# Kernel tuning notes

Measured on AMD Instinct MI355X. Metric: run time of the kernel, lower is better.

## Reference

```python
import jax, jax.numpy as jnp
import numpy as np

B, H, N, D = 8, 12, 1024, 64
SCALE = 1.0 / float(np.sqrt(D))  # 0.125; torch forward default is 1.0 but 1/sqrt(d) is the production value
EPS = 1e-06


def setup_inputs() -> dict:
    key = jax.random.key(0)
    kq, kk, kv = jax.random.split(key, 3)
    q = jax.random.normal(kq, (B, H, N, D), dtype=jnp.float32)
    k = jax.random.normal(kk, (B, H, N, D), dtype=jnp.float32)
    v = jax.random.normal(kv, (B, H, N, D), dtype=jnp.float32)
    # Parameter init per L2Q.__init__: alpha=0.125, beta=0.5, gamma=1/n_tokens
    alpha = jnp.full((H, 1, 1), 0.125, dtype=jnp.float32)
    beta = jnp.full((H, 1, 1), 0.5, dtype=jnp.float32)
    gamma = jnp.full((H, 1, 1), 1.0 / N, dtype=jnp.float32)
    return {"q": q, "k": k, "v": v, "alpha": alpha, "beta": beta, "gamma": gamma}


def reference(q, k, v, alpha, beta, gamma):
    # logits: (B, H, N, N)
    logits = jnp.einsum("bhnd,bhmd->bhnm", q, k) * SCALE
    # per-head quadratic polynomial, then ReLU; params (H,1,1) broadcast over (B,H,N,N)
    attn = jax.nn.relu(alpha * logits * logits + beta * logits + gamma)
    attn = attn / (jnp.sum(attn, axis=-1, keepdims=True) + EPS)
    return jnp.einsum("bhnm,bhmd->bhnd", attn, v)
```

## Files before the change

kernel.cpp:

```cpp
#include <hip/hip_runtime.h>
#include <hip/hip_bf16.h>

typedef __attribute__((ext_vector_type(8))) short bf16x8;
typedef __attribute__((ext_vector_type(4))) float f32x4;
typedef __attribute__((ext_vector_type(16))) float f32x16;

#define MFMA16(a, b, c) __builtin_amdgcn_mfma_f32_16x16x32_bf16(a, b, c, 0, 0, 0)
#define MFMA32(a, b, c) __builtin_amdgcn_mfma_f32_32x32x16_bf16(a, b, c, 0, 0, 0)

static constexpr int kH = 12;
static constexpr int kN = 1024;
static constexpr int kD = 64;
static constexpr int kBH = 96;
static constexpr int kND = kN * kD;
static constexpr float kScale = 0.125f;
static constexpr float kEps = 1e-6f;
static constexpr long kTensorElems = (long)kBH * kND;
static constexpr long kWsNeeded = 2 * kTensorElems * 2;

__device__ __forceinline__ unsigned bfbits(float x) {
    union { __hip_bfloat16 h; unsigned short u; } c;
    c.h = __float2bfloat16(x);
    return (unsigned)c.u;
}
__device__ __forceinline__ unsigned pack2_rne(float a, float b) {
    return bfbits(a) | (bfbits(b) << 16);
}
__device__ __forceinline__ unsigned pack2_rhu(float lo, float hi) {
    unsigned a = __builtin_bit_cast(unsigned, lo) + 0x8000u;
    unsigned b = __builtin_bit_cast(unsigned, hi) + 0x8000u;
    return __builtin_amdgcn_perm(b, a, 0x07060302u);
}
__device__ __forceinline__ void gl_lds16(const void* g, void* l) {
    __builtin_amdgcn_global_load_lds(
        (const __attribute__((address_space(1))) void*)g,
        (__attribute__((address_space(3))) void*)l, 16, 0, 0);
}

__global__ __launch_bounds__(256, 2) void prep(
    const float* __restrict__ k, const float* __restrict__ v,
    unsigned* __restrict__ kbf, unsigned* __restrict__ vtb)
{
    static constexpr int TS = 68;
    __shared__ float T32[64 * TS];
    const int bid = blockIdx.x;
    const int bh = bid >> 4, nt = bid & 15;
    const int t = threadIdx.x;

    const float* kp = k + (long)bh * kND + (long)nt * 64 * kD;
    unsigned* ko = kbf + ((long)bh * kND + (long)nt * 64 * kD) / 2;
#pragma unroll
    for (int r = 0; r < 4; ++r) {
        const int f4 = t + 256 * r;
        const float4 f = ((const float4*)kp)[f4];
        uint2 u;
        u.x = pack2_rne(f.x, f.y);
        u.y = pack2_rne(f.z, f.w);
        *(uint2*)&ko[f4 * 2] = u;
    }

    const float* vp = v + (long)bh * kND + (long)nt * 64 * kD;
#pragma unroll
    for (int r = 0; r < 4; ++r) {
        const int f4 = t + 256 * r;
        const int n = f4 >> 4, d4 = f4 & 15;
        const float4 f = *(const float4*)(vp + (long)n * kD + 4 * d4);
        *(float4*)&T32[n * TS + 4 * d4] = f;
    }
    __syncthreads();
    const int d = t >> 2, c = t & 3;
    unsigned u[8];
#pragma unroll
    for (int j = 0; j < 8; ++j) {
        const int key = c * 16 + 2 * j;
        u[j] = pack2_rne(T32[key * TS + d], T32[(key + 1) * TS + d]);
    }
    unsigned* dst = vtb + (long)bh * (kND / 2) + (long)d * (kN / 2) + nt * 32 + c * 8;
    uint4 A, B;
    A.x = u[0]; A.y = u[1]; A.z = u[4]; A.w = u[5];
    B.x = u[2]; B.y = u[3]; B.z = u[6]; B.w = u[7];
    *(uint4*)(dst)     = A;
    *(uint4*)(dst + 4) = B;
}

__global__ __launch_bounds__(256, 3) void l2q_main(
    const float* __restrict__ q,
    const unsigned short* __restrict__ kbf, const unsigned short* __restrict__ vtbf,
    const float* __restrict__ alpha, const float* __restrict__ beta, const float* __restrict__ gamma,
    float* __restrict__ out)
{
    __shared__ __align__(16) unsigned Ks[2][2048];
    __shared__ __align__(16) unsigned Vs[2][2048];

    const int bid  = blockIdx.x;
    const int xcd  = bid & 7;
    const int sIdx = bid >> 3;
    const int bh   = xcd * 12 + (sIdx % 12);
    const int qt   = sIdx / 12;
    const int h    = bh % kH;
    const int t    = threadIdx.x;
    const int wave = t >> 6;
    const int lane = t & 63;
    const int l31  = lane & 31;
    const int hh   = lane >> 5;

    const float al = alpha[h] * (kScale * kScale);
    const float be = beta[h] * kScale;
    const float ga = gamma[h];

    const float* qp = q + (long)bh * kND;
    const unsigned short* kp = kbf + (long)bh * kND;
    const unsigned short* vp = vtbf + (long)bh * kND;

    bf16x8 qbF[4];
    {
        const int qrow = qt * 128 + wave * 32 + l31;
        const float* qsrc = qp + (long)qrow * kD;
#pragma unroll
        for (int s = 0; s < 4; ++s) {
            const float4 f0 = *(const float4*)(qsrc + s * 16 + hh * 8);
            const float4 f1 = *(const float4*)(qsrc + s * 16 + hh * 8 + 4);
            uint4 u;
            u.x = pack2_rne(f0.x, f0.y);
            u.y = pack2_rne(f0.z, f0.w);
            u.z = pack2_rne(f1.x, f1.y);
            u.w = pack2_rne(f1.z, f1.w);
            qbF[s] = __builtin_bit_cast(bf16x8, u);
        }
    }

    f32x16 oacc[2];
#pragma unroll
    for (int db = 0; db < 2; ++db)
#pragma unroll
        for (int r = 0; r < 16; ++r)
            oacc[db][r] = 0.f;
    float dacc[4] = {0.f, 0.f, 0.f, 0.f};

    const int srow8 = lane >> 3;
    const int g8    = lane & 7;
    auto stageKV = [&](int buf, int tile) {
        const int k0 = tile * 64;
#pragma unroll
        for (int c = 0; c < 2; ++c) {
            const int r = (c * 4 + wave) * 8 + srow8;
            gl_lds16(kp + (long)(k0 + r) * kD + (g8 ^ srow8) * 8, &Ks[buf][(c * 4 + wave) * 256]);
            gl_lds16(vp + (long)r * kN + k0 + (g8 ^ srow8) * 8, &Vs[buf][(c * 4 + wave) * 256]);
        }
    };

    stageKV(0, 0);

    for (int tile = 0; tile < 16; ++tile) {
        const int buf = tile & 1;
        __syncthreads();
        if (tile + 1 < 16) stageKV(buf ^ 1, tile + 1);

        const unsigned* Kb = Ks[buf];
        const unsigned* Vb = Vs[buf];

        f32x16 st[2];
#pragma unroll
        for (int kb = 0; kb < 2; ++kb)
#pragma unroll
            for (int r = 0; r < 16; ++r)
                st[kb][r] = 0.f;
#pragma unroll
        for (int s = 0; s < 4; ++s) {
            const int g = (s << 1) | hh;
#pragma unroll
            for (int kb = 0; kb < 2; ++kb) {
                const int row = kb * 32 + l31;
                bf16x8 ka = *(const bf16x8*)&Kb[row * 32 + ((g ^ (row & 7)) << 2)];
                st[kb] = MFMA32(ka, qbF[s], st[kb]);
            }
        }

        bf16x8 vfr[2][4];
#pragma unroll
        for (int db = 0; db < 2; ++db) {
            const int row = db * 32 + l31;
            const int rb = row * 32;
            const int rsw = row & 7;
#pragma unroll
            for (int s = 0; s < 4; ++s)
                vfr[db][s] = *(const bf16x8*)&Vb[rb + ((((s << 1) | hh) ^ rsw) << 2)];
        }

        unsigned u[2][8];
#pragma unroll
        for (int kb = 0; kb < 2; ++kb) {
#pragma unroll
            for (int p = 0; p < 8; ++p) {
                const float s0 = st[kb][2 * p], s1 = st[kb][2 * p + 1];
                const float w0 = fmaxf(fmaf(fmaf(al, s0, be), s0, ga), 0.f);
                const float w1 = fmaxf(fmaf(fmaf(al, s1, be), s1, ga), 0.f);
                dacc[p & 3] += w0 + w1;
                u[kb][p] = pack2_rhu(w0, w1);
            }
        }

#pragma unroll
        for (int s = 0; s < 4; ++s) {
            uint4 fr;
            const int kb = s >> 1, b = (s & 1) * 4;
            fr.x = u[kb][b + 0];
            fr.y = u[kb][b + 1];
            fr.z = u[kb][b + 2];
            fr.w = u[kb][b + 3];
            const bf16x8 pa = __builtin_bit_cast(bf16x8, fr);
            oacc[0] = MFMA32(pa, vfr[0][s], oacc[0]);
            oacc[1] = MFMA32(pa, vfr[1][s], oacc[1]);
        }
    }

    float d = (dacc[0] + dacc[1]) + (dacc[2] + dacc[3]);
    d += __shfl_xor(d, 32);
    const float inv = 1.0f / (d + kEps);

    const long obase = (long)bh * kND;
    const int rowbase = qt * 128 + wave * 32;
#pragma unroll
    for (int r = 0; r < 16; ++r) {
        const int row32 = (r & 3) + 8 * (r >> 2) + 4 * hh;
        const float iv = __shfl(inv, row32);
        float* o = out + obase + (long)(rowbase + row32) * kD + l31;
        o[0]  = oacc[0][r] * iv;
        o[32] = oacc[1][r] * iv;
    }
}

static constexpr int KSU = 36;
static constexpr int VSU = 36;
static constexpr int PSU = 36;

__global__ __launch_bounds__(256, 3) void l2q_attn_fb(
    const float* __restrict__ q, const float* __restrict__ k, const float* __restrict__ v,
    const float* __restrict__ alpha, const float* __restrict__ beta, const float* __restrict__ gamma,
    float* __restrict__ out)
{
    __shared__ __align__(16) unsigned KsU[64 * KSU];
    __shared__ __align__(16) unsigned VtU[64 * VSU];
    __shared__ __align__(16) unsigned PU[128 * PSU];

    const int bid  = blockIdx.x;
    const int bh   = bid >> 3;
    const int qt   = bid & 7;
    const int h    = bh % kH;
    const int t    = threadIdx.x;
    const int wave = t >> 6;
    const int lane = t & 63;
    const int quad = lane >> 4;
    const int l15  = lane & 15;

    const float al = alpha[h], be = beta[h], ga = gamma[h];

    const long base = (long)bh * kN * kD;
    const float* qp = q + base;
    const float* kp = k + base;
    const float* vp = v + base;

    bf16x8 qa[2][2];
#pragma unroll
    for (int rb = 0; rb < 2; ++rb) {
        const int row = qt * 128 + wave * 32 + rb * 16 + l15;
#pragma unroll
        for (int kc = 0; kc < 2; ++kc) {
            const float* src = qp + (long)row * kD + kc * 32 + quad * 8;
            const float4 f0 = *(const float4*)(src);
            const float4 f1 = *(const float4*)(src + 4);
            uint4 u;
            u.x = pack2_rne(f0.x, f0.y);
            u.y = pack2_rne(f0.z, f0.w);
            u.z = pack2_rne(f1.x, f1.y);
            u.w = pack2_rne(f1.z, f1.w);
            qa[rb][kc] = __builtin_bit_cast(bf16x8, u);
        }
    }

    f32x4 oacc[2][4];
#pragma unroll
    for (int rb = 0; rb < 2; ++rb)
#pragma unroll
        for (int db = 0; db < 4; ++db)
            oacc[rb][db] = (f32x4){0.f, 0.f, 0.f, 0.f};

    float dsum[2][4] = {{0.f, 0.f, 0.f, 0.f}, {0.f, 0.f, 0.f, 0.f}};
    unsigned* Pw = &PU[wave * 32 * PSU];

    for (int tile = 0; tile < 16; ++tile) {
        __syncthreads();
        const int k0 = tile * 64;
#pragma unroll
        for (int r = 0; r < 4; ++r) {
            const int f4 = t + 256 * r;
            const int n = f4 >> 4, d4 = f4 & 15;
            const float4 kg = *(const float4*)(kp + (long)(k0 + n) * kD + 4 * d4);
            uint2 pk;
            pk.x = pack2_rne(kg.x, kg.y);
            pk.y = pack2_rne(kg.z, kg.w);
            *(uint2*)&KsU[n * KSU + 2 * d4] = pk;
        }
#pragma unroll
        for (int r = 0; r < 2; ++r) {
            const int u = t + 256 * r;
            const int key2 = u & 31, d4 = u >> 5;
            const float* s0 = vp + (long)(k0 + 2 * key2) * kD + 4 * d4;
            const float4 va = *(const float4*)(s0);
            const float4 vb = *(const float4*)(s0 + kD);
            VtU[(4 * d4 + 0) * VSU + key2] = pack2_rne(va.x, vb.x);
            VtU[(4 * d4 + 1) * VSU + key2] = pack2_rne(va.y, vb.y);
            VtU[(4 * d4 + 2) * VSU + key2] = pack2_rne(va.z, vb.z);
            VtU[(4 * d4 + 3) * VSU + key2] = pack2_rne(va.w, vb.w);
        }
        __syncthreads();

        f32x4 s[2][4];
#pragma unroll
        for (int rb = 0; rb < 2; ++rb)
#pragma unroll
            for (int nb = 0; nb < 4; ++nb)
                s[rb][nb] = (f32x4){0.f, 0.f, 0.f, 0.f};
#pragma unroll
        for (int nb = 0; nb < 4; ++nb) {
            bf16x8 kb0 = *(const bf16x8*)&KsU[(nb * 16 + l15) * KSU + 4 * quad];
            bf16x8 kb1 = *(const bf16x8*)&KsU[(nb * 16 + l15) * KSU + 16 + 4 * quad];
#pragma unroll
            for (int rb = 0; rb < 2; ++rb) {
                s[rb][nb] = MFMA16(qa[rb][0], kb0, s[rb][nb]);
                s[rb][nb] = MFMA16(qa[rb][1], kb1, s[rb][nb]);
            }
        }

        const bool ev = (lane & 1) == 0;
#pragma unroll
        for (int rb = 0; rb < 2; ++rb) {
#pragma unroll
            for (int nb = 0; nb < 4; ++nb) {
                float w0, w1, w2, w3;
                {
                    float l0 = s[rb][nb][0] * kScale;
                    float l1 = s[rb][nb][1] * kScale;
                    float l2 = s[rb][nb][2] * kScale;
                    float l3 = s[rb][nb][3] * kScale;
                    w0 = fmaxf(fmaf(fmaf(al, l0, be), l0, ga), 0.f);
                    w1 = fmaxf(fmaf(fmaf(al, l1, be), l1, ga), 0.f);
                    w2 = fmaxf(fmaf(fmaf(al, l2, be), l2, ga), 0.f);
                    w3 = fmaxf(fmaf(fmaf(al, l3, be), l3, ga), 0.f);
                }
                dsum[rb][0] += w0; dsum[rb][1] += w1;
                dsum[rb][2] += w2; dsum[rb][3] += w3;

                const float o0 = __shfl_xor(w0, 1);
                const float o1 = __shfl_xor(w1, 1);
                const float o2 = __shfl_xor(w2, 1);
                const float o3 = __shfl_xor(w3, 1);
                const unsigned pa = ev ? pack2_rne(w0, o0) : pack2_rne(o2, w2);
                const unsigned pb = ev ? pack2_rne(w1, o1) : pack2_rne(o3, w3);
                const int r0 = ev ? 0 : 2;
                const int cu = (16 * nb + (l15 & ~1)) >> 1;
                const int rowb = rb * 16 + quad * 4 + r0;
                Pw[rowb * PSU + cu] = pa;
                Pw[(rowb + 1) * PSU + cu] = pb;
            }
        }

        bf16x8 pf[2][2];
#pragma unroll
        for (int rb = 0; rb < 2; ++rb)
#pragma unroll
            for (int kc = 0; kc < 2; ++kc)
                pf[rb][kc] = *(const bf16x8*)&Pw[(rb * 16 + l15) * PSU + 16 * kc + 4 * quad];
#pragma unroll
        for (int db = 0; db < 4; ++db) {
            bf16x8 vf0 = *(const bf16x8*)&VtU[(db * 16 + l15) * VSU + 4 * quad];
            bf16x8 vf1 = *(const bf16x8*)&VtU[(db * 16 + l15) * VSU + 16 + 4 * quad];
#pragma unroll
            for (int rb = 0; rb < 2; ++rb) {
                oacc[rb][db] = MFMA16(pf[rb][0], vf0, oacc[rb][db]);
                oacc[rb][db] = MFMA16(pf[rb][1], vf1, oacc[rb][db]);
            }
        }
    }

#pragma unroll
    for (int rb = 0; rb < 2; ++rb)
#pragma unroll
        for (int i = 0; i < 4; ++i) {
            float d = dsum[rb][i];
            d += __shfl_xor(d, 1);
            d += __shfl_xor(d, 2);
            d += __shfl_xor(d, 4);
            d += __shfl_xor(d, 8);
            dsum[rb][i] = 1.0f / (d + kEps);
        }

#pragma unroll
    for (int rb = 0; rb < 2; ++rb)
#pragma unroll
        for (int db = 0; db < 4; ++db)
#pragma unroll
            for (int i = 0; i < 4; ++i) {
                const int row = qt * 128 + wave * 32 + rb * 16 + quad * 4 + i;
                out[base + (long)row * kD + db * 16 + l15] = oacc[rb][db][i] * dsum[rb][i];
            }
}

extern "C" void kernel_launch(void* const* d_in, const int* in_sizes, int n_in,
                              void* d_out, int out_size, void* d_ws, size_t ws_size,
                              hipStream_t stream) {
    const float* q     = (const float*)d_in[0];
    const float* k     = (const float*)d_in[1];
    const float* v     = (const float*)d_in[2];
    const float* alpha = (const float*)d_in[3];
    const float* beta  = (const float*)d_in[4];
    const float* gamma = (const float*)d_in[5];
    float* out = (float*)d_out;

    if (ws_size < (size_t)kWsNeeded) {
        l2q_attn_fb<<<dim3(768), dim3(256), 0, stream>>>(q, k, v, alpha, beta, gamma, out);
        return;
    }

    unsigned* kbf = (unsigned*)d_ws;
    unsigned* vtb = kbf + kTensorElems / 2;

    prep<<<dim3(1536), dim3(256), 0, stream>>>(k, v, kbf, vtb);
    l2q_main<<<dim3(768), dim3(256), 0, stream>>>(
        q, (const unsigned short*)kbf, (const unsigned short*)vtb,
        alpha, beta, gamma, out);
}
```

Measured before the change: 144.3 us.

## Software-pipeline QK^T of next tile with PV of current tile

Restructures the key loop so the QK^T MFMAs for tile t+1 are issued right after the polynomial weights of tile t are formed, interleaved with that tile's PV MFMAs. V staging moves to a three-deep LDS buffer, and loads are prefetched two tiles ahead while K stays double-buffered. The loop is wrapped in s_setprio to favour the MFMA-heavy section. The aim is to hide the dependency between the score MFMAs and the elementwise/pack work, and to hide load latency. In exchange it uses more LDS (extra V buffer) and keeps the score accumulators live across iterations, which raises register pressure.

```diff
diff --git a/kernel.cpp b/kernel.cpp
--- a/kernel.cpp
+++ b/kernel.cpp
@@ -90,7 +90,7 @@
     float* __restrict__ out)
 {
     __shared__ __align__(16) unsigned Ks[2][2048];
-    __shared__ __align__(16) unsigned Vs[2][2048];
+    __shared__ __align__(16) unsigned Vs[3][2048];
 
     const int bid  = blockIdx.x;
     const int xcd  = bid & 7;
@@ -139,27 +139,26 @@
 
     const int srow8 = lane >> 3;
     const int g8    = lane & 7;
-    auto stageKV = [&](int buf, int tile) {
+    auto stageKV = [&](int tile) {
+        const int kbuf = tile & 1;
+        const int vbuf = tile % 3;
         const int k0 = tile * 64;
 #pragma unroll
         for (int c = 0; c < 2; ++c) {
-            const int r = (c * 4 + wave) * 8 + srow8;
-            gl_lds16(kp + (long)(k0 + r) * kD + (g8 ^ srow8) * 8, &Ks[buf][(c * 4 + wave) * 256]);
-            gl_lds16(vp + (long)r * kN + k0 + (g8 ^ srow8) * 8, &Vs[buf][(c * 4 + wave) * 256]);
+            const int seg = c * 4 + wave;
+            const int r = seg * 8 + srow8;
+            gl_lds16(kp + (long)(k0 + r) * kD + (g8 ^ srow8) * 8, &Ks[kbuf][seg * 256]);
+            gl_lds16(vp + (long)r * kN + k0 + (g8 ^ srow8) * 8, &Vs[vbuf][seg * 256]);
         }
     };
 
-    stageKV(0, 0);
-
-    for (int tile = 0; tile < 16; ++tile) {
-        const int buf = tile & 1;
-        __syncthreads();
-        if (tile + 1 < 16) stageKV(buf ^ 1, tile + 1);
-
-        const unsigned* Kb = Ks[buf];
-        const unsigned* Vb = Vs[buf];
-
-        f32x16 st[2];
+    stageKV(0);
+    stageKV(1);
+    __syncthreads();
+
+    f32x16 st[2];
+    {
+        const unsigned* Kb = Ks[0];
 #pragma unroll
         for (int kb = 0; kb < 2; ++kb)
 #pragma unroll
@@ -175,7 +174,13 @@
                 st[kb] = MFMA32(ka, qbF[s], st[kb]);
             }
         }
-
+    }
+
+    for (int tile = 0; tile < 16; ++tile) {
+        __syncthreads();
+        if (tile + 2 < 16) stageKV(tile + 2);
+
+        const unsigned* Vb = Vs[tile % 3];
         bf16x8 vfr[2][4];
 #pragma unroll
         for (int db = 0; db < 2; ++db) {
@@ -197,6 +202,26 @@
                 const float w1 = fmaxf(fmaf(fmaf(al, s1, be), s1, ga), 0.f);
                 dacc[p & 3] += w0 + w1;
                 u[kb][p] = pack2_rhu(w0, w1);
+            }
+        }
+
+        __builtin_amdgcn_s_setprio(1);
+        if (tile + 1 < 16) {
+            const unsigned* Kb = Ks[(tile + 1) & 1];
+#pragma unroll
+            for (int kb = 0; kb < 2; ++kb)
+#pragma unroll
+                for (int r = 0; r < 16; ++r)
+                    st[kb][r] = 0.f;
+#pragma unroll
+            for (int s = 0; s < 4; ++s) {
+                const int g = (s << 1) | hh;
+#pragma unroll
+                for (int kb = 0; kb < 2; ++kb) {
+                    const int row = kb * 32 + l31;
+                    bf16x8 ka = *(const bf16x8*)&Kb[row * 32 + ((g ^ (row & 7)) << 2)];
+                    st[kb] = MFMA32(ka, qbF[s], st[kb]);
+                }
             }
         }
 
@@ -212,6 +237,7 @@
             oacc[0] = MFMA32(pa, vfr[0][s], oacc[0]);
             oacc[1] = MFMA32(pa, vfr[1][s], oacc[1]);
         }
+        __builtin_amdgcn_s_setprio(0);
     }
 
     float d = (dacc[0] + dacc[1]) + (dacc[2] + dacc[3]);
```

After: 152.6 us. 5.8% more time.

## Pre-swizzle V into MFMA fragment layout and load directly from global

Applied to the files above, without the earlier changes.

The V-transpose prep kernel now writes V^T in a fragment-ordered layout, so each lane's bf16x8 MFMA operand is contiguous in global memory. The main kernel drops the V LDS double buffer and loads V fragments straight from global (L2) into registers at the start of each tile, before the QK MFMAs. This removes LDS staging traffic and LDS footprint for V, which could raise occupancy. The cost is exposed global-load latency inside the loop, with no async prefetch beyond issuing the loads before the score computation.

```diff
diff --git a/kernel.cpp b/kernel.cpp
--- a/kernel.cpp
+++ b/kernel.cpp
@@ -75,12 +75,13 @@
         const int key = c * 16 + 2 * j;
         u[j] = pack2_rne(T32[key * TS + d], T32[(key + 1) * TS + d]);
     }
-    unsigned* dst = vtb + (long)bh * (kND / 2) + (long)d * (kN / 2) + nt * 32 + c * 8;
     uint4 A, B;
     A.x = u[0]; A.y = u[1]; A.z = u[4]; A.w = u[5];
     B.x = u[2]; B.y = u[3]; B.z = u[6]; B.w = u[7];
-    *(uint4*)(dst)     = A;
-    *(uint4*)(dst + 4) = B;
+    unsigned* vbase = vtb + (long)bh * (kND / 2);
+    const long o0 = (long)nt * 2048 + ((d >> 5) * 4 + c) * 256 + (d & 31) * 4;
+    *(uint4*)(vbase + o0)       = A;
+    *(uint4*)(vbase + o0 + 128) = B;
 }
 
 __global__ __launch_bounds__(256, 3) void l2q_main(
@@ -90,7 +91,6 @@
     float* __restrict__ out)
 {
     __shared__ __align__(16) unsigned Ks[2][2048];
-    __shared__ __align__(16) unsigned Vs[2][2048];
 
     const int bid  = blockIdx.x;
     const int xcd  = bid & 7;
@@ -110,7 +110,7 @@
 
     const float* qp = q + (long)bh * kND;
     const unsigned short* kp = kbf + (long)bh * kND;
-    const unsigned short* vp = vtbf + (long)bh * kND;
+    const unsigned* vlin = (const unsigned*)vtbf + (long)bh * (kND / 2);
 
     bf16x8 qbF[4];
     {
@@ -139,25 +139,32 @@
 
     const int srow8 = lane >> 3;
     const int g8    = lane & 7;
-    auto stageKV = [&](int buf, int tile) {
+    auto stageK = [&](int buf, int tile) {
         const int k0 = tile * 64;
 #pragma unroll
         for (int c = 0; c < 2; ++c) {
-            const int r = (c * 4 + wave) * 8 + srow8;
-            gl_lds16(kp + (long)(k0 + r) * kD + (g8 ^ srow8) * 8, &Ks[buf][(c * 4 + wave) * 256]);
-            gl_lds16(vp + (long)r * kN + k0 + (g8 ^ srow8) * 8, &Vs[buf][(c * 4 + wave) * 256]);
+            const int seg = c * 4 + wave;
+            const int r = seg * 8 + srow8;
+            gl_lds16(kp + (long)(k0 + r) * kD + (g8 ^ srow8) * 8, &Ks[buf][seg * 256]);
         }
     };
 
-    stageKV(0, 0);
+    stageK(0, 0);
 
     for (int tile = 0; tile < 16; ++tile) {
         const int buf = tile & 1;
         __syncthreads();
-        if (tile + 1 < 16) stageKV(buf ^ 1, tile + 1);
+        if (tile + 1 < 16) stageK(buf ^ 1, tile + 1);
+
+        const unsigned* vt0 = vlin + (long)tile * 2048 + (hh * 32 + l31) * 4;
+        bf16x8 vfr[2][4];
+#pragma unroll
+        for (int db = 0; db < 2; ++db)
+#pragma unroll
+            for (int s = 0; s < 4; ++s)
+                vfr[db][s] = *(const bf16x8*)(vt0 + (db * 4 + s) * 256);
 
         const unsigned* Kb = Ks[buf];
-        const unsigned* Vb = Vs[buf];
 
         f32x16 st[2];
 #pragma unroll
@@ -174,17 +181,6 @@
                 bf16x8 ka = *(const bf16x8*)&Kb[row * 32 + ((g ^ (row & 7)) << 2)];
                 st[kb] = MFMA32(ka, qbF[s], st[kb]);
             }
-        }
-
-        bf16x8 vfr[2][4];
-#pragma unroll
-        for (int db = 0; db < 2; ++db) {
-            const int row = db * 32 + l31;
-            const int rb = row * 32;
-            const int rsw = row & 7;
-#pragma unroll
-            for (int s = 0; s < 4; ++s)
-                vfr[db][s] = *(const bf16x8*)&Vb[rb + ((((s << 1) | hh) ^ rsw) << 2)];
         }
 
         unsigned u[2][8];
```

New measurement: 145.3 us. No clear change (+0.8%).
